# Optimization experiments

Hardware: AMD Instinct MI355X
Metric: run time of the kernel (lower is better)

Reference implementation:

```python
import jax, jax.numpy as jnp
import numpy as np

D_MODEL, D_INNER, D_STATE, DT_RANK, K = 768, 1536, 16, 48, 4
B, L = 2, 1024


def causal_depthwise_conv(x, w, b):
    # x: [B, L, D], w: [D, 1, K], b: [D]; torch pads K-1 both sides then slices [:L] -> causal left pad
    xt = x.transpose(0, 2, 1)  # [B, D, L]
    out = jax.lax.conv_general_dilated(
        xt, w, window_strides=(1,), padding=[(K - 1, 0)],
        dimension_numbers=('NCH', 'OIH', 'NCH'), feature_group_count=xt.shape[1])
    return out.transpose(0, 2, 1) + b


def ssm(xc, A_log, D, W_dt, dtW, dtb, W_B, W_C):
    # xc: [B, L, Din]
    A = -jnp.exp(A_log)                                   # [Din, N]
    dt_low = jnp.einsum('bld,rd->blr', xc, W_dt)          # [B, L, R]
    delta = jax.nn.softplus(jnp.einsum('blr,dr->bld', dt_low, dtW) + dtb)  # [B, L, Din]
    Bm = jnp.einsum('bld,nd->bln', xc, W_B)               # [B, L, N]
    Cm = jnp.einsum('bld,nd->bln', xc, W_C)               # [B, L, N]
    deltaA = jnp.exp(delta[..., None] * A)                # [B, L, Din, N]
    BX = (delta * xc)[..., None] * Bm[:, :, None, :]      # [B, L, Din, N]

    def combine(e1, e2):
        a1, b1 = e1
        a2, b2 = e2
        return a1 * a2, a2 * b1 + b2

    _, hs = jax.lax.associative_scan(combine, (deltaA, BX), axis=1)  # [B, L, Din, N]
    y = jnp.einsum('bldn,bln->bld', hs, Cm) + D * xc
    return y


def setup_inputs() -> dict:
    key = jax.random.key(0)
    ks = jax.random.split(key, 20)
    s = 0.02
    A_init = jnp.log(jnp.broadcast_to(jnp.arange(1, D_STATE + 1, dtype=jnp.float32), (D_INNER, D_STATE)))
    return {
        'x': jax.random.normal(ks[0], (B, L, D_MODEL), jnp.float32),
        'W_in_states': jax.random.normal(ks[1], (D_INNER, D_MODEL), jnp.float32) * s,
        'W_in_gates': jax.random.normal(ks[2], (D_INNER, D_MODEL), jnp.float32) * s,
        'conv_w': jax.random.normal(ks[3], (D_INNER, 1, K), jnp.float32) * 0.2,
        'conv_b': jax.random.normal(ks[4], (D_INNER,), jnp.float32) * 0.02,
        'conv_w_b': jax.random.normal(ks[5], (D_INNER, 1, K), jnp.float32) * 0.2,
        'conv_b_b': jax.random.normal(ks[6], (D_INNER,), jnp.float32) * 0.02,
        'W_dt': jax.random.normal(ks[7], (DT_RANK, D_INNER), jnp.float32) * s,
        'W_B': jax.random.normal(ks[8], (D_STATE, D_INNER), jnp.float32) * s,
        'W_C': jax.random.normal(ks[9], (D_STATE, D_INNER), jnp.float32) * s,
        'dtW': jax.random.normal(ks[10], (D_INNER, DT_RANK), jnp.float32) * s,
        'dtb': jax.random.normal(ks[11], (D_INNER,), jnp.float32) * 0.1,
        'A_log': A_init,
        'Dp': jnp.ones((D_INNER,), jnp.float32),
        'W_dt_b': jax.random.normal(ks[12], (DT_RANK, D_INNER), jnp.float32) * s,
        'W_B_b': jax.random.normal(ks[13], (D_STATE, D_INNER), jnp.float32) * s,
        'W_C_b': jax.random.normal(ks[14], (D_STATE, D_INNER), jnp.float32) * s,
        'dtW_b': jax.random.normal(ks[15], (D_INNER, DT_RANK), jnp.float32) * s,
        'dtb_b': jax.random.normal(ks[16], (D_INNER,), jnp.float32) * 0.1,
        'A_log_b': A_init,
        'Dp_b': jnp.ones((D_INNER,), jnp.float32),
        'W_out': jax.random.normal(ks[17], (D_MODEL, D_INNER), jnp.float32) * s,
    }


def reference(x, W_in_states, W_in_gates, conv_w, conv_b, conv_w_b, conv_b_b,
              W_dt, W_B, W_C, dtW, dtb, A_log, Dp,
              W_dt_b, W_B_b, W_C_b, dtW_b, dtb_b, A_log_b, Dp_b, W_out):
    xs = jnp.einsum('blm,dm->bld', x, W_in_states)  # [B, L, Din]
    z = jnp.einsum('blm,dm->bld', x, W_in_gates)    # [B, L, Din]
    # forward branch
    xc = jax.nn.silu(causal_depthwise_conv(xs, conv_w, conv_b))
    y = ssm(xc, A_log, Dp, W_dt, dtW, dtb, W_B, W_C)
    # backward branch: xz flipped along L, split -> reversed xs / reversed z
    xs_b = xs[:, ::-1]
    z_b = z[:, ::-1]
    xcb = jax.nn.silu(causal_depthwise_conv(xs_b, conv_w_b, conv_b_b))
    y_b = ssm(xcb, A_log_b, Dp_b, W_dt_b, dtW_b, dtb_b, W_B_b, W_C_b)
    # gating
    y = y * jax.nn.silu(z)
    y_b = y_b * jax.nn.silu(z_b)
    y = (y + y_b[:, ::-1]) * 0.5  # divide_output
    return jnp.einsum('bld,md->blm', y, W_out)
```

## Files before the change

kernel.cpp:

```cpp
#include <hip/hip_runtime.h>
#include <hip/hip_bf16.h>
#include <stdint.h>

#define DM 768
#define DI 1536
#define DSTATE 16
#define RNK 48
#define BB 2
#define LL 1024
#define ML (BB * LL)

#define NSEG 32
#define SEGL (LL / NSEG)

#define PROJ_NCHUNK 8
#define PROJ_KC (DI / PROJ_NCHUNK)

typedef unsigned short u16;
typedef __bf16 bf16x8 __attribute__((ext_vector_type(8)));
typedef float f32x4 __attribute__((ext_vector_type(4)));

struct __align__(8) u16x4_t { u16 x, y, z, w; };

__device__ __forceinline__ float b2f(u16 u) {
  union { uint32_t i; float f; } v; v.i = ((uint32_t)u) << 16; return v.f;
}
__device__ __forceinline__ u16 f2b(float f) {
  union { float f; uint32_t i; } v; v.f = f;
  uint32_t r = v.i + 0x7FFFu + ((v.i >> 16) & 1u);
  return (u16)(r >> 16);
}
__device__ __forceinline__ float silu_f(float x) { return x / (1.f + __expf(-x)); }
__device__ __forceinline__ float softplus_f(float s) {
  return fmaxf(s, 0.f) + __logf(1.f + __expf(-fabsf(s)));
}
__device__ __forceinline__ u16x4_t cvt4(float4 v) {
  u16x4_t o; o.x = f2b(v.x); o.y = f2b(v.y); o.z = f2b(v.z); o.w = f2b(v.w); return o;
}

__device__ __forceinline__ void gl16(const u16* g, u16* l) {
  __builtin_amdgcn_global_load_lds(
      (const __attribute__((address_space(1))) uint32_t*)g,
      (__attribute__((address_space(3))) uint32_t*)l, 16, 0, 0);
}

#define SEG_X    (ML * DM / 4)
#define SEG_W    (DI * DM / 4)
#define SEG_CAT  (128 * DI / 4)
#define SEG_DTW  (DI * 64 / 4)
__global__ __launch_bounds__(256) void convert_kernel(
    const float4* __restrict__ x, const float4* __restrict__ wis,
    const float4* __restrict__ wig, const float4* __restrict__ wout,
    const float* __restrict__ W_B, const float* __restrict__ W_C,
    const float* __restrict__ W_dt,
    const float* __restrict__ W_B_b, const float* __restrict__ W_C_b,
    const float* __restrict__ W_dt_b,
    const float* __restrict__ dtW, const float* __restrict__ dtW_b,
    u16x4_t* __restrict__ xb, u16x4_t* __restrict__ wisb,
    u16x4_t* __restrict__ wigb, u16x4_t* __restrict__ woutb,
    u16x4_t* __restrict__ wcf, u16x4_t* __restrict__ wcb,
    u16x4_t* __restrict__ dtwf, u16x4_t* __restrict__ dtwb)
{
  int idx = blockIdx.x * 256 + threadIdx.x;
  if (idx < SEG_X) { xb[idx] = cvt4(x[idx]); return; }
  idx -= SEG_X;
  if (idx < SEG_W) { wisb[idx] = cvt4(wis[idx]); return; }
  idx -= SEG_W;
  if (idx < SEG_W) { wigb[idx] = cvt4(wig[idx]); return; }
  idx -= SEG_W;
  if (idx < SEG_W) { woutb[idx] = cvt4(wout[idx]); return; }
  idx -= SEG_W;
  if (idx < 2 * SEG_CAT) {
    int dir = idx / SEG_CAT;
    int rem = idx % SEG_CAT;
    int row = rem / (DI / 4), k4 = rem % (DI / 4);
    const float* src = nullptr;
    if (row < 16)      src = (dir ? W_B_b  : W_B)  + (size_t)row * DI + k4 * 4;
    else if (row < 32) src = (dir ? W_C_b  : W_C)  + (size_t)(row - 16) * DI + k4 * 4;
    else if (row < 80) src = (dir ? W_dt_b : W_dt) + (size_t)(row - 32) * DI + k4 * 4;
    u16x4_t o;
    if (src) o = cvt4(*(const float4*)src);
    else { o.x = 0; o.y = 0; o.z = 0; o.w = 0; }
    (dir ? wcb : wcf)[rem] = o;
    return;
  }
  idx -= 2 * SEG_CAT;
  int dir = idx / SEG_DTW;
  int rem = idx % SEG_DTW;
  int d = rem / 16, r4 = rem % 16;
  const float* Dw = dir ? dtW_b : dtW;
  u16x4_t o;
  if (r4 < 12) o = cvt4(*(const float4*)(Dw + (size_t)d * RNK + r4 * 4));
  else { o.x = 0; o.y = 0; o.z = 0; o.w = 0; }
  (dir ? dtwb : dtwf)[rem] = o;
}

__global__ __launch_bounds__(256) void gemm_bt(
    const u16* __restrict__ A, const u16* __restrict__ B0,
    const u16* __restrict__ B1, int Nsplit,
    void* __restrict__ Cout, int M, int N, int K, int ldc, int epi,
    const u16* __restrict__ A2, const u16* __restrict__ B2,
    void* __restrict__ C2,
    const float* __restrict__ ebias, const float* __restrict__ ebias2)
{
  if (blockIdx.z) { A = A2; B0 = B2; Cout = C2; ebias = ebias2; }
  __shared__ alignas(16) u16 As[2][128 * 32];
  __shared__ alignas(16) u16 Bs[2][128 * 32];
  const int tid = threadIdx.x;
  const int wave = tid >> 6, lane = tid & 63;
  const int bm = blockIdx.y * 128;
  const int bn = blockIdx.x * 128;

  const u16* Bmat = B0;
  int ncol0 = bn;
  int epi_l = epi;
  if (B1 != nullptr && bn >= Nsplit) { Bmat = B1; ncol0 = bn - Nsplit; epi_l = 1; }

  const int c0 = tid, c1 = tid + 256;
  const u16* gA0 = A + (size_t)(bm + (c0 >> 2)) * K + (c0 & 3) * 8;
  const u16* gA1 = A + (size_t)(bm + (c1 >> 2)) * K + (c1 & 3) * 8;
  const u16* gB0 = Bmat + (size_t)(ncol0 + (c0 >> 2)) * K + (c0 & 3) * 8;
  const u16* gB1 = Bmat + (size_t)(ncol0 + (c1 >> 2)) * K + (c1 & 3) * 8;

  const int wm = (wave & 1) * 64, wn = (wave >> 1) * 64;
  const int rl = lane & 15, q = lane >> 4;

  f32x4 acc[4][4];
#pragma unroll
  for (int i = 0; i < 4; ++i)
#pragma unroll
    for (int j = 0; j < 4; ++j) acc[i][j] = (f32x4){0.f, 0.f, 0.f, 0.f};

  auto stage = [&](int buf, int k0) {
    gl16(gA0 + k0, &As[buf][c0 * 8]);
    gl16(gA1 + k0, &As[buf][c1 * 8]);
    gl16(gB0 + k0, &Bs[buf][c0 * 8]);
    gl16(gB1 + k0, &Bs[buf][c1 * 8]);
  };

  stage(0, 0);
  __syncthreads();
  int cur = 0;
  for (int k0 = 0; k0 < K; k0 += 32) {
    const bool more = (k0 + 32 < K);
    if (more) stage(cur ^ 1, k0 + 32);

    const bf16x8* AsV = (const bf16x8*)As[cur];
    const bf16x8* BsV = (const bf16x8*)Bs[cur];
    bf16x8 af[4], bfv[4];
#pragma unroll
    for (int s = 0; s < 4; ++s) {
      af[s]  = AsV[(wm + s * 16 + rl) * 4 + q];
      bfv[s] = BsV[(wn + s * 16 + rl) * 4 + q];
    }
#pragma unroll
    for (int i = 0; i < 4; ++i)
#pragma unroll
      for (int j = 0; j < 4; ++j)
        acc[i][j] = __builtin_amdgcn_mfma_f32_16x16x32_bf16(af[i], bfv[j], acc[i][j], 0, 0, 0);

    if (more) {
      __syncthreads();
      cur ^= 1;
    }
  }

#pragma unroll
  for (int i = 0; i < 4; ++i) {
#pragma unroll
    for (int j = 0; j < 4; ++j) {
#pragma unroll
      for (int r = 0; r < 4; ++r) {
        int row = bm + wm + i * 16 + q * 4 + r;
        int col = bn + wn + j * 16 + rl;
        float v = acc[i][j][r];
        if (epi_l == 1) v = silu_f(v);
        if (epi == 6) {
          ((u16*)Cout)[(size_t)row * ldc + col] = f2b(softplus_f(v + ebias[col]));
        } else {
          ((u16*)Cout)[(size_t)row * ldc + col] = f2b(v);
        }
      }
    }
  }
}

__global__ __launch_bounds__(256) void gemm_proj_sk(
    const u16* __restrict__ xcf, const u16* __restrict__ xcb,
    const u16* __restrict__ wcf, const u16* __restrict__ wcb,
    float* __restrict__ part)
{
  const int dir = blockIdx.z;
  const u16* A = dir ? xcb : xcf;
  const u16* B = dir ? wcb : wcf;
  const int kc = blockIdx.x;
  const int bm = blockIdx.y * 128;
  const int kbase = kc * PROJ_KC;

  __shared__ alignas(16) u16 As[128 * 32];
  __shared__ alignas(16) u16 Bs[128 * 32];
  const int tid = threadIdx.x;
  const int wave = tid >> 6, lane = tid & 63;
  const int c0 = tid, c1 = tid + 256;
  const u16* gA0 = A + (size_t)(bm + (c0 >> 2)) * DI + kbase + (c0 & 3) * 8;
  const u16* gA1 = A + (size_t)(bm + (c1 >> 2)) * DI + kbase + (c1 & 3) * 8;
  const u16* gB0 = B + (size_t)(c0 >> 2) * DI + kbase + (c0 & 3) * 8;
  const u16* gB1 = B + (size_t)(c1 >> 2) * DI + kbase + (c1 & 3) * 8;
  uint4* lA0 = (uint4*)&As[c0 * 8]; uint4* lA1 = (uint4*)&As[c1 * 8];
  uint4* lB0 = (uint4*)&Bs[c0 * 8]; uint4* lB1 = (uint4*)&Bs[c1 * 8];

  const int wm = (wave & 1) * 64, wn = (wave >> 1) * 64;
  const int rl = lane & 15, q = lane >> 4;

  f32x4 acc[4][4];
#pragma unroll
  for (int i = 0; i < 4; ++i)
#pragma unroll
    for (int j = 0; j < 4; ++j) acc[i][j] = (f32x4){0.f, 0.f, 0.f, 0.f};

  const bf16x8* AsV = (const bf16x8*)As;
  const bf16x8* BsV = (const bf16x8*)Bs;

  uint4 ra0 = *(const uint4*)(gA0);
  uint4 ra1 = *(const uint4*)(gA1);
  uint4 rb0 = *(const uint4*)(gB0);
  uint4 rb1 = *(const uint4*)(gB1);

  for (int k0 = 0; k0 < PROJ_KC; k0 += 32) {
    *lA0 = ra0; *lA1 = ra1; *lB0 = rb0; *lB1 = rb1;
    __syncthreads();
    if (k0 + 32 < PROJ_KC) {
      ra0 = *(const uint4*)(gA0 + k0 + 32);
      ra1 = *(const uint4*)(gA1 + k0 + 32);
      rb0 = *(const uint4*)(gB0 + k0 + 32);
      rb1 = *(const uint4*)(gB1 + k0 + 32);
    }
    bf16x8 af[4], bfv[4];
#pragma unroll
    for (int s = 0; s < 4; ++s) {
      af[s]  = AsV[(wm + s * 16 + rl) * 4 + q];
      bfv[s] = BsV[(wn + s * 16 + rl) * 4 + q];
    }
#pragma unroll
    for (int i = 0; i < 4; ++i)
#pragma unroll
      for (int j = 0; j < 4; ++j)
        acc[i][j] = __builtin_amdgcn_mfma_f32_16x16x32_bf16(af[i], bfv[j], acc[i][j], 0, 0, 0);
    __syncthreads();
  }

  float* pout = part + ((size_t)(dir * PROJ_NCHUNK + kc) * ML + bm) * 128;
#pragma unroll
  for (int i = 0; i < 4; ++i) {
#pragma unroll
    for (int j = 0; j < 4; ++j) {
#pragma unroll
      for (int r = 0; r < 4; ++r) {
        int row = wm + i * 16 + q * 4 + r;
        int col = wn + j * 16 + rl;
        pout[(size_t)row * 128 + col] = acc[i][j][r];
      }
    }
  }
}

__global__ __launch_bounds__(256) void proj_reduce(
    const float* __restrict__ part,
    float* __restrict__ pf, float* __restrict__ pb,
    u16* __restrict__ dtlf, u16* __restrict__ dtlb)
{
  int idx = blockIdx.x * 256 + threadIdx.x;
  int col = idx % 96;
  int t = idx / 96;
  int row = t % ML;
  int dir = t / ML;
  const float* p = part + ((size_t)dir * PROJ_NCHUNK * ML + row) * 128 + col;
  float s = 0.f;
#pragma unroll
  for (int c = 0; c < PROJ_NCHUNK; ++c)
    s += p[(size_t)c * ML * 128];
  if (col < 32) (dir ? pb : pf)[(size_t)row * 32 + col] = s;
  else          (dir ? dtlb : dtlf)[(size_t)row * 64 + (col - 32)] = f2b(s);
}

__global__ __launch_bounds__(256) void gemm_out64(
    const u16* __restrict__ A, const u16* __restrict__ Bw,
    float* __restrict__ out)
{
  __shared__ alignas(16) u16 As[64 * 72];
  __shared__ alignas(16) u16 Bs[64 * 72];
  const int tid = threadIdx.x;
  const int wave = tid >> 6, lane = tid & 63;
  const int bm = blockIdx.y * 64;
  const int bn = blockIdx.x * 64;

  const int c0 = tid, c1 = tid + 256;
  const u16* gA0 = A + (size_t)(bm + (c0 >> 3)) * DI + (c0 & 7) * 8;
  const u16* gA1 = A + (size_t)(bm + (c1 >> 3)) * DI + (c1 & 7) * 8;
  const u16* gB0 = Bw + (size_t)(bn + (c0 >> 3)) * DI + (c0 & 7) * 8;
  const u16* gB1 = Bw + (size_t)(bn + (c1 >> 3)) * DI + (c1 & 7) * 8;
  uint4* lA0 = (uint4*)&As[(c0 >> 3) * 72 + (c0 & 7) * 8];
  uint4* lA1 = (uint4*)&As[(c1 >> 3) * 72 + (c1 & 7) * 8];
  uint4* lB0 = (uint4*)&Bs[(c0 >> 3) * 72 + (c0 & 7) * 8];
  uint4* lB1 = (uint4*)&Bs[(c1 >> 3) * 72 + (c1 & 7) * 8];

  const int rl = lane & 15, q = lane >> 4;

  f32x4 acc[4];
#pragma unroll
  for (int s = 0; s < 4; ++s) acc[s] = (f32x4){0.f, 0.f, 0.f, 0.f};

  uint4 ra0 = *(const uint4*)gA0, ra1 = *(const uint4*)gA1;
  uint4 rb0 = *(const uint4*)gB0, rb1 = *(const uint4*)gB1;

  for (int k0 = 0; k0 < DI; k0 += 64) {
    *lA0 = ra0; *lA1 = ra1; *lB0 = rb0; *lB1 = rb1;
    __syncthreads();
    if (k0 + 64 < DI) {
      ra0 = *(const uint4*)(gA0 + k0 + 64);
      ra1 = *(const uint4*)(gA1 + k0 + 64);
      rb0 = *(const uint4*)(gB0 + k0 + 64);
      rb1 = *(const uint4*)(gB1 + k0 + 64);
    }
    bf16x8 bf[2], af;
#pragma unroll
    for (int c = 0; c < 2; ++c)
      bf[c] = *(const bf16x8*)&Bs[(wave * 16 + rl) * 72 + c * 32 + q * 8];
#pragma unroll
    for (int s = 0; s < 4; ++s) {
#pragma unroll
      for (int c = 0; c < 2; ++c) {
        af = *(const bf16x8*)&As[(s * 16 + rl) * 72 + c * 32 + q * 8];
        acc[s] = __builtin_amdgcn_mfma_f32_16x16x32_bf16(af, bf[c], acc[s], 0, 0, 0);
      }
    }
    __syncthreads();
  }

#pragma unroll
  for (int s = 0; s < 4; ++s) {
#pragma unroll
    for (int r = 0; r < 4; ++r) {
      int row = bm + s * 16 + q * 4 + r;
      int col = bn + wave * 16 + rl;
      out[(size_t)row * DM + col] = acc[s][r];
    }
  }
}

__global__ void conv_kernel(
    const u16* __restrict__ xsg,
    const float* __restrict__ cw, const float* __restrict__ cb,
    const float* __restrict__ cwb, const float* __restrict__ cbb,
    u16* __restrict__ xc, u16* __restrict__ xcb)
{
  int idx = blockIdx.x * 256 + threadIdx.x;
  int d = idx % DI;
  int row = idx / DI;
  int l = row % LL, b = row / LL;
  const u16* base = xsg + (size_t)b * LL * 3072 + d;

  float4 wf = *(const float4*)(cw + d * 4);
  float4 wb = *(const float4*)(cwb + d * 4);
  float wfk[4] = {wf.x, wf.y, wf.z, wf.w};
  float wbk[4] = {wb.x, wb.y, wb.z, wb.w};

  float accf = cb[d];
  float accb = cbb[d];
#pragma unroll
  for (int k = 0; k < 4; ++k) {
    int ls = l - 3 + k;
    if (ls >= 0) {
      accf += wfk[k] * b2f(base[(size_t)ls * 3072]);
      accb += wbk[k] * b2f(base[(size_t)(LL - 1 - ls) * 3072]);
    }
  }
  xc[idx]  = f2b(silu_f(accf));
  xcb[idx] = f2b(silu_f(accb));
}

__global__ void combine_kernel(
    const u16* __restrict__ ybr, const u16* __restrict__ xsg, u16* yf)
{
  int idx = blockIdx.x * 256 + threadIdx.x;
  int d = idx % DI;
  int row = idx / DI;
  int l = row % LL, b = row / LL;
  float g = b2f(xsg[(size_t)row * 3072 + DI + d]);
  float vb = b2f(ybr[((size_t)b * LL + (LL - 1 - l)) * DI + d]);
  float v = 0.5f * (b2f(yf[idx]) + vb) * g;
  yf[idx] = f2b(v);
}

__global__ __launch_bounds__(256) void scan_sum(
    const u16* __restrict__ df, const u16* __restrict__ db,
    const u16* __restrict__ xcf, const u16* __restrict__ xcb,
    const float* __restrict__ pf, const float* __restrict__ pb,
    const float* __restrict__ A_log, const float* __restrict__ A_log_b,
    float* __restrict__ sdl, float* __restrict__ bs)
{
  const int dir = blockIdx.z / NSEG, seg = blockIdx.z % NSEG;
  const u16* delta = dir ? db : df;
  const u16* xc = dir ? xcb : xcf;
  const float* proj = dir ? pb : pf;
  const float* Al = dir ? A_log_b : A_log;
  const int b = blockIdx.y;
  const int d = blockIdx.x * 256 + threadIdx.x;
  const int l0 = seg * SEGL;

  __shared__ float Bsh[SEGL][16];
  for (int i = threadIdx.x; i < SEGL * 16; i += 256) {
    int l = i >> 4, n = i & 15;
    Bsh[l][n] = proj[((size_t)b * LL + l0 + l) * 32 + n];
  }
  __syncthreads();

  float An[16];
#pragma unroll
  for (int n = 0; n < 16; ++n) An[n] = -__expf(Al[d * 16 + n]);

  float h[16];
#pragma unroll
  for (int n = 0; n < 16; ++n) h[n] = 0.f;
  float S = 0.f;

  const u16* dbase = delta + ((size_t)b * LL + l0) * DI + d;
  const u16* xbase = xc + ((size_t)b * LL + l0) * DI + d;

  for (int g = 0; g < SEGL; g += 4) {
    float dl4[4], dx4[4];
#pragma unroll
    for (int j = 0; j < 4; ++j) {
      float dv = b2f(dbase[(size_t)(g + j) * DI]);
      float xv = b2f(xbase[(size_t)(g + j) * DI]);
      dl4[j] = dv; dx4[j] = dv * xv;
    }
#pragma unroll
    for (int j = 0; j < 4; ++j) {
      S += dl4[j];
#pragma unroll
      for (int n = 0; n < 16; ++n)
        h[n] = __expf(dl4[j] * An[n]) * h[n] + dx4[j] * Bsh[g + j][n];
    }
  }

  size_t base = (((size_t)dir * BB + b) * NSEG + seg) * DI + d;
  sdl[base] = S;
#pragma unroll
  for (int n = 0; n < 16; ++n) bs[base * 16 + n] = h[n];
}

__global__ __launch_bounds__(256) void scan_carry(
    const float* __restrict__ A_log, const float* __restrict__ A_log_b,
    const float* __restrict__ sdl, float* __restrict__ bs)
{
  int idx = blockIdx.x * 256 + threadIdx.x;
  int n = idx & 15;
  int t = idx >> 4;
  int d = t % DI;
  int b = (t / DI) % BB;
  int dir = t / (DI * BB);
  const float* Al = dir ? A_log_b : A_log;
  float An = -__expf(Al[d * 16 + n]);
  float h = 0.f;
  for (int s = 0; s < NSEG; ++s) {
    size_t base = (((size_t)dir * BB + b) * NSEG + s) * DI + d;
    float S = sdl[base];
    float bv = bs[base * 16 + n];
    bs[base * 16 + n] = h;
    h = __expf(S * An) * h + bv;
  }
}

__global__ __launch_bounds__(256) void scan_apply(
    const u16* __restrict__ df, const u16* __restrict__ db,
    const u16* __restrict__ xcf, const u16* __restrict__ xcb,
    const float* __restrict__ pf, const float* __restrict__ pb,
    const float* __restrict__ A_log, const float* __restrict__ A_log_b,
    const float* __restrict__ Dp, const float* __restrict__ Dp_b,
    const float* __restrict__ bs,
    u16* __restrict__ y_f, u16* __restrict__ y_b)
{
  const int dir = blockIdx.z / NSEG, seg = blockIdx.z % NSEG;
  const u16* delta = dir ? db : df;
  const u16* xc = dir ? xcb : xcf;
  const float* proj = dir ? pb : pf;
  const float* Al = dir ? A_log_b : A_log;
  const float* Dpp = dir ? Dp_b : Dp;
  u16* y = dir ? y_b : y_f;
  const int b = blockIdx.y;
  const int d = blockIdx.x * 256 + threadIdx.x;
  const int l0 = seg * SEGL;

  __shared__ float BCsh[SEGL][32];
  for (int i = threadIdx.x; i < SEGL * 32; i += 256) {
    int l = i >> 5, j = i & 31;
    BCsh[l][j] = proj[((size_t)b * LL + l0 + l) * 32 + j];
  }
  __syncthreads();

  float An[16];
#pragma unroll
  for (int n = 0; n < 16; ++n) An[n] = -__expf(Al[d * 16 + n]);
  const float Dv = Dpp[d];

  float h[16];
  size_t cbase = (((size_t)dir * BB + b) * NSEG + seg) * DI + d;
#pragma unroll
  for (int n = 0; n < 16; ++n) h[n] = bs[cbase * 16 + n];

  const u16* dbase = delta + ((size_t)b * LL + l0) * DI + d;
  const u16* xbase = xc + ((size_t)b * LL + l0) * DI + d;
  u16* ybase = y + ((size_t)b * LL + l0) * DI + d;

  for (int g = 0; g < SEGL; g += 4) {
    float dl4[4], xv4[4];
#pragma unroll
    for (int j = 0; j < 4; ++j) {
      dl4[j] = b2f(dbase[(size_t)(g + j) * DI]);
      xv4[j] = b2f(xbase[(size_t)(g + j) * DI]);
    }
#pragma unroll
    for (int j = 0; j < 4; ++j) {
      float dx = dl4[j] * xv4[j];
      float yv = 0.f;
#pragma unroll
      for (int n = 0; n < 16; ++n) {
        h[n] = __expf(dl4[j] * An[n]) * h[n] + dx * BCsh[g + j][n];
        yv += h[n] * BCsh[g + j][16 + n];
      }
      ybase[(size_t)(g + j) * DI] = f2b(yv + Dv * xv4[j]);
    }
  }
}

extern "C" void kernel_launch(void* const* d_in, const int* in_sizes, int n_in,
                              void* d_out, int out_size, void* d_ws, size_t ws_size,
                              hipStream_t stream)
{
  const float* x       = (const float*)d_in[0];
  const float* Wis     = (const float*)d_in[1];
  const float* Wig     = (const float*)d_in[2];
  const float* conv_w  = (const float*)d_in[3];
  const float* conv_b  = (const float*)d_in[4];
  const float* conv_wb = (const float*)d_in[5];
  const float* conv_bb = (const float*)d_in[6];
  const float* W_dt    = (const float*)d_in[7];
  const float* W_B     = (const float*)d_in[8];
  const float* W_C     = (const float*)d_in[9];
  const float* dtW     = (const float*)d_in[10];
  const float* dtb     = (const float*)d_in[11];
  const float* A_log   = (const float*)d_in[12];
  const float* Dp      = (const float*)d_in[13];
  const float* W_dt_b  = (const float*)d_in[14];
  const float* W_B_b   = (const float*)d_in[15];
  const float* W_C_b   = (const float*)d_in[16];
  const float* dtW_b   = (const float*)d_in[17];
  const float* dtb_b   = (const float*)d_in[18];
  const float* A_log_b = (const float*)d_in[19];
  const float* Dp_b    = (const float*)d_in[20];
  const float* W_out   = (const float*)d_in[21];

  char* ws = (char*)d_ws;
  size_t off = 0;
  auto alloc = [&](size_t bytes) -> char* {
    char* p = ws + off; off += (bytes + 255) & ~(size_t)255; return p;
  };
  u16*   xb    = (u16*)alloc((size_t)ML * DM * 2);
  u16*   wisb  = (u16*)alloc((size_t)DI * DM * 2);
  u16*   wigb  = (u16*)alloc((size_t)DI * DM * 2);
  u16*   woutb = (u16*)alloc((size_t)DM * DI * 2);
  u16*   xsg = (u16*)alloc((size_t)ML * 3072 * 2);
  u16*   xc  = (u16*)alloc((size_t)ML * DI * 2);
  u16*   xcb = (u16*)alloc((size_t)ML * DI * 2);
  u16*   wcf = (u16*)alloc((size_t)128 * DI * 2);
  u16*   wcb = (u16*)alloc((size_t)128 * DI * 2);
  u16*   dtwf = (u16*)alloc((size_t)DI * 64 * 2);
  u16*   dtwb = (u16*)alloc((size_t)DI * 64 * 2);
  float* pf  = (float*)alloc((size_t)ML * 32 * 4);
  float* pb  = (float*)alloc((size_t)ML * 32 * 4);
  u16*   dtlf = (u16*)alloc((size_t)ML * 64 * 2);
  u16*   dtlb = (u16*)alloc((size_t)ML * 64 * 2);
  u16*   df  = (u16*)alloc((size_t)ML * DI * 2);
  u16*   db  = (u16*)alloc((size_t)ML * DI * 2);
  u16*   yf  = (u16*)alloc((size_t)ML * DI * 2);
  u16*   ybr = (u16*)alloc((size_t)ML * DI * 2);
  float* sdl = (float*)alloc((size_t)2 * BB * NSEG * DI * 4);
  float* bs  = (float*)alloc((size_t)2 * BB * NSEG * DI * 16 * 4);
  float* part = (float*)alloc((size_t)2 * PROJ_NCHUNK * ML * 128 * 4);

  const int conv_total = SEG_X + 3 * SEG_W + 2 * SEG_CAT + 2 * SEG_DTW;
  convert_kernel<<<(conv_total + 255) / 256, 256, 0, stream>>>(
      (const float4*)x, (const float4*)Wis, (const float4*)Wig, (const float4*)W_out,
      W_B, W_C, W_dt, W_B_b, W_C_b, W_dt_b, dtW, dtW_b,
      (u16x4_t*)xb, (u16x4_t*)wisb, (u16x4_t*)wigb, (u16x4_t*)woutb,
      (u16x4_t*)wcf, (u16x4_t*)wcb, (u16x4_t*)dtwf, (u16x4_t*)dtwb);

  gemm_bt<<<dim3(3072 / 128, ML / 128, 1), 256, 0, stream>>>(
      xb, wisb, wigb, DI, xsg, ML, 3072, DM, 3072, 0,
      nullptr, nullptr, nullptr, nullptr, nullptr);

  conv_kernel<<<(ML * DI) / 256, 256, 0, stream>>>(
      xsg, conv_w, conv_b, conv_wb, conv_bb, xc, xcb);

  gemm_proj_sk<<<dim3(PROJ_NCHUNK, ML / 128, 2), 256, 0, stream>>>(
      xc, xcb, wcf, wcb, part);
  proj_reduce<<<(2 * ML * 96) / 256, 256, 0, stream>>>(
      part, pf, pb, dtlf, dtlb);

  gemm_bt<<<dim3(DI / 128, ML / 128, 2), 256, 0, stream>>>(
      dtlf, dtwf, nullptr, 1 << 30, df, ML, DI, 64, DI, 6,
      dtlb, dtwb, db, dtb, dtb_b);

  scan_sum<<<dim3(DI / 256, BB, 2 * NSEG), 256, 0, stream>>>(
      df, db, xc, xcb, pf, pb, A_log, A_log_b, sdl, bs);
  scan_carry<<<(2 * BB * DI * 16) / 256, 256, 0, stream>>>(
      A_log, A_log_b, sdl, bs);
  scan_apply<<<dim3(DI / 256, BB, 2 * NSEG), 256, 0, stream>>>(
      df, db, xc, xcb, pf, pb, A_log, A_log_b, Dp, Dp_b, bs, yf, ybr);

  combine_kernel<<<(ML * DI) / 256, 256, 0, stream>>>(ybr, xsg, yf);

  gemm_out64<<<dim3(DM / 64, ML / 64, 1), 256, 0, stream>>>(
      yf, woutb, (float*)d_out);
}
```

Baseline: 265.6 us.

## Fuse bidirectional scan apply with gating combine; widen GEMM K-tile to 64

Forward and backward scan-apply now run in one kernel, so `combine_kernel` can be removed. Each block first computes the forward segment into an LDS buffer, then computes the mirrored backward segment. It applies the gate and averaging and writes the combined output directly. This removes the yf/ybr intermediate writes and the separate combine pass, but halves the grid and serializes the two directions inside each block. Separately, the general bf16 GEMM stages 64-wide K tiles instead of 32, which halves barriers per K but doubles LDS use to 64KB and may cost occupancy or add bank conflicts.

```diff
diff --git a/kernel.cpp b/kernel.cpp
--- a/kernel.cpp
+++ b/kernel.cpp
@@ -104,8 +104,8 @@
     const float* __restrict__ ebias, const float* __restrict__ ebias2)
 {
   if (blockIdx.z) { A = A2; B0 = B2; Cout = C2; ebias = ebias2; }
-  __shared__ alignas(16) u16 As[2][128 * 32];
-  __shared__ alignas(16) u16 Bs[2][128 * 32];
+  __shared__ alignas(16) u16 As[2][128 * 64];
+  __shared__ alignas(16) u16 Bs[2][128 * 64];
   const int tid = threadIdx.x;
   const int wave = tid >> 6, lane = tid & 63;
   const int bm = blockIdx.y * 128;
@@ -116,11 +116,14 @@
   int epi_l = epi;
   if (B1 != nullptr && bn >= Nsplit) { Bmat = B1; ncol0 = bn - Nsplit; epi_l = 1; }
 
-  const int c0 = tid, c1 = tid + 256;
-  const u16* gA0 = A + (size_t)(bm + (c0 >> 2)) * K + (c0 & 3) * 8;
-  const u16* gA1 = A + (size_t)(bm + (c1 >> 2)) * K + (c1 & 3) * 8;
-  const u16* gB0 = Bmat + (size_t)(ncol0 + (c0 >> 2)) * K + (c0 & 3) * 8;
-  const u16* gB1 = Bmat + (size_t)(ncol0 + (c1 >> 2)) * K + (c1 & 3) * 8;
+  const u16* gA[4]; const u16* gB[4]; int cs[4];
+#pragma unroll
+  for (int i = 0; i < 4; ++i) {
+    int c = tid + i * 256;
+    cs[i] = c;
+    gA[i] = A + (size_t)(bm + (c >> 3)) * K + (c & 7) * 8;
+    gB[i] = Bmat + (size_t)(ncol0 + (c >> 3)) * K + (c & 7) * 8;
+  }
 
   const int wm = (wave & 1) * 64, wn = (wave >> 1) * 64;
   const int rl = lane & 15, q = lane >> 4;
@@ -132,32 +135,34 @@
     for (int j = 0; j < 4; ++j) acc[i][j] = (f32x4){0.f, 0.f, 0.f, 0.f};
 
   auto stage = [&](int buf, int k0) {
-    gl16(gA0 + k0, &As[buf][c0 * 8]);
-    gl16(gA1 + k0, &As[buf][c1 * 8]);
-    gl16(gB0 + k0, &Bs[buf][c0 * 8]);
-    gl16(gB1 + k0, &Bs[buf][c1 * 8]);
+#pragma unroll
+    for (int i = 0; i < 4; ++i) {
+      gl16(gA[i] + k0, &As[buf][cs[i] * 8]);
+      gl16(gB[i] + k0, &Bs[buf][cs[i] * 8]);
+    }
   };
 
   stage(0, 0);
   __syncthreads();
   int cur = 0;
-  for (int k0 = 0; k0 < K; k0 += 32) {
-    const bool more = (k0 + 32 < K);
-    if (more) stage(cur ^ 1, k0 + 32);
-
-    const bf16x8* AsV = (const bf16x8*)As[cur];
-    const bf16x8* BsV = (const bf16x8*)Bs[cur];
-    bf16x8 af[4], bfv[4];
-#pragma unroll
-    for (int s = 0; s < 4; ++s) {
-      af[s]  = AsV[(wm + s * 16 + rl) * 4 + q];
-      bfv[s] = BsV[(wn + s * 16 + rl) * 4 + q];
-    }
-#pragma unroll
-    for (int i = 0; i < 4; ++i)
-#pragma unroll
-      for (int j = 0; j < 4; ++j)
-        acc[i][j] = __builtin_amdgcn_mfma_f32_16x16x32_bf16(af[i], bfv[j], acc[i][j], 0, 0, 0);
+  for (int k0 = 0; k0 < K; k0 += 64) {
+    const bool more = (k0 + 64 < K);
+    if (more) stage(cur ^ 1, k0 + 64);
+
+#pragma unroll
+    for (int kk = 0; kk < 2; ++kk) {
+      bf16x8 af[4], bfv[4];
+#pragma unroll
+      for (int s = 0; s < 4; ++s) {
+        af[s]  = *(const bf16x8*)&As[cur][(wm + s * 16 + rl) * 64 + kk * 32 + q * 8];
+        bfv[s] = *(const bf16x8*)&Bs[cur][(wn + s * 16 + rl) * 64 + kk * 32 + q * 8];
+      }
+#pragma unroll
+      for (int i = 0; i < 4; ++i)
+#pragma unroll
+        for (int j = 0; j < 4; ++j)
+          acc[i][j] = __builtin_amdgcn_mfma_f32_16x16x32_bf16(af[i], bfv[j], acc[i][j], 0, 0, 0);
+    }
 
     if (more) {
       __syncthreads();
@@ -377,19 +382,6 @@
   }
   xc[idx]  = f2b(silu_f(accf));
   xcb[idx] = f2b(silu_f(accb));
-}
-
-__global__ void combine_kernel(
-    const u16* __restrict__ ybr, const u16* __restrict__ xsg, u16* yf)
-{
-  int idx = blockIdx.x * 256 + threadIdx.x;
-  int d = idx % DI;
-  int row = idx / DI;
-  int l = row % LL, b = row / LL;
-  float g = b2f(xsg[(size_t)row * 3072 + DI + d]);
-  float vb = b2f(ybr[((size_t)b * LL + (LL - 1 - l)) * DI + d]);
-  float v = 0.5f * (b2f(yf[idx]) + vb) * g;
-  yf[idx] = f2b(v);
 }
 
 __global__ __launch_bounds__(256) void scan_sum(
@@ -472,64 +464,110 @@
   }
 }
 
-__global__ __launch_bounds__(256) void scan_apply(
+__global__ __launch_bounds__(256) void scan_apply2(
     const u16* __restrict__ df, const u16* __restrict__ db,
     const u16* __restrict__ xcf, const u16* __restrict__ xcb,
     const float* __restrict__ pf, const float* __restrict__ pb,
     const float* __restrict__ A_log, const float* __restrict__ A_log_b,
     const float* __restrict__ Dp, const float* __restrict__ Dp_b,
-    const float* __restrict__ bs,
-    u16* __restrict__ y_f, u16* __restrict__ y_b)
-{
-  const int dir = blockIdx.z / NSEG, seg = blockIdx.z % NSEG;
-  const u16* delta = dir ? db : df;
-  const u16* xc = dir ? xcb : xcf;
-  const float* proj = dir ? pb : pf;
-  const float* Al = dir ? A_log_b : A_log;
-  const float* Dpp = dir ? Dp_b : Dp;
-  u16* y = dir ? y_b : y_f;
+    const float* __restrict__ bs, const u16* __restrict__ xsg,
+    u16* __restrict__ yc)
+{
+  const int s = blockIdx.z;
   const int b = blockIdx.y;
   const int d = blockIdx.x * 256 + threadIdx.x;
-  const int l0 = seg * SEGL;
 
   __shared__ float BCsh[SEGL][32];
-  for (int i = threadIdx.x; i < SEGL * 32; i += 256) {
-    int l = i >> 5, j = i & 31;
-    BCsh[l][j] = proj[((size_t)b * LL + l0 + l) * 32 + j];
-  }
-  __syncthreads();
-
-  float An[16];
-#pragma unroll
-  for (int n = 0; n < 16; ++n) An[n] = -__expf(Al[d * 16 + n]);
-  const float Dv = Dpp[d];
-
-  float h[16];
-  size_t cbase = (((size_t)dir * BB + b) * NSEG + seg) * DI + d;
-#pragma unroll
-  for (int n = 0; n < 16; ++n) h[n] = bs[cbase * 16 + n];
-
-  const u16* dbase = delta + ((size_t)b * LL + l0) * DI + d;
-  const u16* xbase = xc + ((size_t)b * LL + l0) * DI + d;
-  u16* ybase = y + ((size_t)b * LL + l0) * DI + d;
-
-  for (int g = 0; g < SEGL; g += 4) {
-    float dl4[4], xv4[4];
-#pragma unroll
-    for (int j = 0; j < 4; ++j) {
-      dl4[j] = b2f(dbase[(size_t)(g + j) * DI]);
-      xv4[j] = b2f(xbase[(size_t)(g + j) * DI]);
-    }
-#pragma unroll
-    for (int j = 0; j < 4; ++j) {
-      float dx = dl4[j] * xv4[j];
-      float yv = 0.f;
-#pragma unroll
-      for (int n = 0; n < 16; ++n) {
-        h[n] = __expf(dl4[j] * An[n]) * h[n] + dx * BCsh[g + j][n];
-        yv += h[n] * BCsh[g + j][16 + n];
-      }
-      ybase[(size_t)(g + j) * DI] = f2b(yv + Dv * xv4[j]);
+  __shared__ u16 yfsh[SEGL][256];
+
+  {
+    const int l0 = s * SEGL;
+    for (int i = threadIdx.x; i < SEGL * 32; i += 256) {
+      int l = i >> 5, j = i & 31;
+      BCsh[l][j] = pf[((size_t)b * LL + l0 + l) * 32 + j];
+    }
+    __syncthreads();
+
+    float An[16];
+#pragma unroll
+    for (int n = 0; n < 16; ++n) An[n] = -__expf(A_log[d * 16 + n]);
+    const float Dv = Dp[d];
+
+    float h[16];
+    size_t cbase = (((size_t)b) * NSEG + s) * DI + d;
+#pragma unroll
+    for (int n = 0; n < 16; ++n) h[n] = bs[cbase * 16 + n];
+
+    const u16* dbase = df + ((size_t)b * LL + l0) * DI + d;
+    const u16* xbase = xcf + ((size_t)b * LL + l0) * DI + d;
+
+    for (int g = 0; g < SEGL; g += 4) {
+      float dl4[4], xv4[4];
+#pragma unroll
+      for (int j = 0; j < 4; ++j) {
+        dl4[j] = b2f(dbase[(size_t)(g + j) * DI]);
+        xv4[j] = b2f(xbase[(size_t)(g + j) * DI]);
+      }
+#pragma unroll
+      for (int j = 0; j < 4; ++j) {
+        float dx = dl4[j] * xv4[j];
+        float yv = 0.f;
+#pragma unroll
+        for (int n = 0; n < 16; ++n) {
+          h[n] = __expf(dl4[j] * An[n]) * h[n] + dx * BCsh[g + j][n];
+          yv += h[n] * BCsh[g + j][16 + n];
+        }
+        yfsh[g + j][threadIdx.x] = f2b(yv + Dv * xv4[j]);
+      }
+    }
+    __syncthreads();
+  }
+
+  {
+    const int seg1 = NSEG - 1 - s;
+    const int l0r = seg1 * SEGL;
+    for (int i = threadIdx.x; i < SEGL * 32; i += 256) {
+      int l = i >> 5, j = i & 31;
+      BCsh[l][j] = pb[((size_t)b * LL + l0r + l) * 32 + j];
+    }
+    __syncthreads();
+
+    float An[16];
+#pragma unroll
+    for (int n = 0; n < 16; ++n) An[n] = -__expf(A_log_b[d * 16 + n]);
+    const float Dv = Dp_b[d];
+
+    float h[16];
+    size_t cbase = (((size_t)BB + b) * NSEG + seg1) * DI + d;
+#pragma unroll
+    for (int n = 0; n < 16; ++n) h[n] = bs[cbase * 16 + n];
+
+    const u16* dbase = db + ((size_t)b * LL + l0r) * DI + d;
+    const u16* xbase = xcb + ((size_t)b * LL + l0r) * DI + d;
+
+    for (int g = 0; g < SEGL; g += 4) {
+      float dl4[4], xv4[4];
+#pragma unroll
+      for (int j = 0; j < 4; ++j) {
+        dl4[j] = b2f(dbase[(size_t)(g + j) * DI]);
+        xv4[j] = b2f(xbase[(size_t)(g + j) * DI]);
+      }
+#pragma unroll
+      for (int j = 0; j < 4; ++j) {
+        float dx = dl4[j] * xv4[j];
+        float yv = 0.f;
+#pragma unroll
+        for (int n = 0; n < 16; ++n) {
+          h[n] = __expf(dl4[j] * An[n]) * h[n] + dx * BCsh[g + j][n];
+          yv += h[n] * BCsh[g + j][16 + n];
+        }
+        yv += Dv * xv4[j];
+        int lrow = 31 - (g + j);
+        int l = s * SEGL + lrow;
+        float gate = b2f(xsg[((size_t)b * LL + l) * 3072 + DI + d]);
+        float out = 0.5f * (b2f(yfsh[lrow][threadIdx.x]) + yv) * gate;
+        yc[((size_t)b * LL + l) * DI + d] = f2b(out);
+      }
     }
   }
 }
@@ -583,8 +621,7 @@
   u16*   dtlb = (u16*)alloc((size_t)ML * 64 * 2);
   u16*   df  = (u16*)alloc((size_t)ML * DI * 2);
   u16*   db  = (u16*)alloc((size_t)ML * DI * 2);
-  u16*   yf  = (u16*)alloc((size_t)ML * DI * 2);
-  u16*   ybr = (u16*)alloc((size_t)ML * DI * 2);
+  u16*   yc  = (u16*)alloc((size_t)ML * DI * 2);
   float* sdl = (float*)alloc((size_t)2 * BB * NSEG * DI * 4);
   float* bs  = (float*)alloc((size_t)2 * BB * NSEG * DI * 16 * 4);
   float* part = (float*)alloc((size_t)2 * PROJ_NCHUNK * ML * 128 * 4);
@@ -616,11 +653,9 @@
       df, db, xc, xcb, pf, pb, A_log, A_log_b, sdl, bs);
   scan_carry<<<(2 * BB * DI * 16) / 256, 256, 0, stream>>>(
       A_log, A_log_b, sdl, bs);
-  scan_apply<<<dim3(DI / 256, BB, 2 * NSEG), 256, 0, stream>>>(
-      df, db, xc, xcb, pf, pb, A_log, A_log_b, Dp, Dp_b, bs, yf, ybr);
-
-  combine_kernel<<<(ML * DI) / 256, 256, 0, stream>>>(ybr, xsg, yf);
+  scan_apply2<<<dim3(DI / 256, BB, NSEG), 256, 0, stream>>>(
+      df, db, xc, xcb, pf, pb, A_log, A_log_b, Dp, Dp_b, bs, xsg, yc);
 
   gemm_out64<<<dim3(DM / 64, ML / 64, 1), 256, 0, stream>>>(
-      yf, woutb, (float*)d_out);
-}
+      yc, woutb, (float*)d_out);
+}
```

After: 270.9 us. Within noise of the previous version (+2.0%).
